# Performance work log

Hardware: AMD Instinct MI355X
Metric: run time of the kernel (lower is better)

Reference implementation:

```python
import jax, jax.numpy as jnp
import numpy as np

B, T, D, H = 64, 128, 256, 256


def setup_inputs() -> dict:
    key = jax.random.key(0)
    k1, k2, k3, k4, k5 = jax.random.split(key, 5)
    inputs = jax.random.normal(k1, (B, T, D), dtype=jnp.float32)
    conditions = jax.random.uniform(k2, (B, T, T), dtype=jnp.float32)
    # Keras GRUCell params (reset_after=True): kernel [D,3H], recurrent_kernel [H,3H], bias [2,3H]
    scale_k = 1.0 / np.sqrt(D)
    scale_r = 1.0 / np.sqrt(H)
    kernel = jax.random.normal(k3, (D, 3 * H), dtype=jnp.float32) * scale_k
    recurrent_kernel = jax.random.normal(k4, (H, 3 * H), dtype=jnp.float32) * scale_r
    bias = jax.random.normal(k5, (2, 3 * H), dtype=jnp.float32) * 0.01
    return {"inputs": inputs, "conditions": conditions, "kernel": kernel,
            "recurrent_kernel": recurrent_kernel, "bias": bias}


def _gru_cell(x, h, kernel, recurrent_kernel, bias):
    # Keras GRUCell, reset_after=True, gate order (z, r, h)
    mx = x @ kernel + bias[0]              # [B, 3H]
    mh = h @ recurrent_kernel + bias[1]    # [B, 3H]
    xz, xr, xh = jnp.split(mx, 3, axis=-1)
    hz, hr, hh = jnp.split(mh, 3, axis=-1)
    z = jax.nn.sigmoid(xz + hz)
    r = jax.nn.sigmoid(xr + hr)
    cand = jnp.tanh(xh + r * hh)
    return z * h + (1.0 - z) * cand


def reference(inputs, conditions, kernel, recurrent_kernel, bias):
    # inputs: [B,T,D]; conditions: [B,T,T]
    x_t = jnp.transpose(inputs, (1, 0, 2))  # [T, B, D]
    units = recurrent_kernel.shape[0]
    b, t = inputs.shape[0], inputs.shape[1]

    def step(outs, i):
        # outs: [T, B, H] outputs so far (zeros for future steps, matching TF TensorArray)
        # next_state[b,:] = sum_j conditions[b,i,j] * outs[j,b,:]
        h_prev = jnp.einsum('bj,jbh->bh', conditions[:, i, :], outs)
        h = _gru_cell(x_t[i], h_prev, kernel, recurrent_kernel, bias)
        outs = outs.at[i].set(h)
        return outs, h

    outs0 = jnp.zeros((t, b, units), dtype=inputs.dtype)
    _, ys = jax.lax.scan(step, outs0, jnp.arange(t))  # ys: [T, B, H]
    return jnp.transpose(ys, (1, 0, 2))  # return_sequences=True -> [B, T, H]
```

## Files before the change

### kernel.cpp

```cpp
#include <hip/hip_runtime.h>
#include <math.h>

#define B 64
#define T 128
#define D 256
#define H 256
#define G3 768

__global__ __launch_bounds__(256) void mx_gemm_kernel(const float* __restrict__ x,
                                                      const float* __restrict__ K,
                                                      const float* __restrict__ bias,
                                                      float* __restrict__ MX) {
    __shared__ float xt[16][D];
    const int r0 = blockIdx.x * 16;
    const int tid = threadIdx.x;

    for (int idx = tid; idx < 16 * D; idx += 256) {
        xt[idx >> 8][idx & 255] = x[(size_t)(r0 + (idx >> 8)) * D + (idx & 255)];
    }
    __syncthreads();

    float acc0[16], acc1[16], acc2[16];
#pragma unroll
    for (int r = 0; r < 16; ++r) { acc0[r] = 0.f; acc1[r] = 0.f; acc2[r] = 0.f; }

    for (int d = 0; d < D; ++d) {
        float k0 = K[(size_t)d * G3 + tid];
        float k1 = K[(size_t)d * G3 + 256 + tid];
        float k2 = K[(size_t)d * G3 + 512 + tid];
#pragma unroll
        for (int r = 0; r < 16; ++r) {
            float xv = xt[r][d];
            acc0[r] += xv * k0;
            acc1[r] += xv * k1;
            acc2[r] += xv * k2;
        }
    }

    float b0 = bias[tid], b1 = bias[256 + tid], b2 = bias[512 + tid];
    for (int r = 0; r < 16; ++r) {
        size_t row = (size_t)(r0 + r) * G3;
        MX[row + tid]       = acc0[r] + b0;
        MX[row + 256 + tid] = acc1[r] + b1;
        MX[row + 512 + tid] = acc2[r] + b2;
    }
}

__global__ __launch_bounds__(1024) void rnn_kernel(const float* __restrict__ cond,
                                                   const float* __restrict__ MX,
                                                   const float* __restrict__ R,
                                                   const float* __restrict__ bias,
                                                   float* __restrict__ out) {
    const int b = blockIdx.x;
    const int tid = threadIdx.x;

    __shared__ float c_row[T];
    __shared__ float hprev[H];
    __shared__ float mh[G3];
    __shared__ float p1[4][H];
    __shared__ float p2[4][G3];
    __shared__ float bias2[G3];

    if (tid < G3) bias2[tid] = bias[G3 + tid];

    const float* condb = cond + (size_t)b * T * T;
    const float* mxb   = MX   + (size_t)b * T * G3;
    float*       outb  = out  + (size_t)b * T * H;
    const float4* R4   = reinterpret_cast<const float4*>(R);

    const int q  = tid >> 8;
    const int h  = tid & 255;
    const int hq = tid / 192;
    const int cg = tid % 192;

    for (int i = 0; i < T; ++i) {
        if (tid < T) c_row[tid] = condb[(size_t)i * T + tid];
        __syncthreads();

        const int len = (i + 3) >> 2;
        const int j0 = q * len;
        const int j1 = min(i, j0 + len);
        float a0 = 0.f, a1 = 0.f, a2 = 0.f, a3 = 0.f;
        int j = j0;
        for (; j + 3 < j1; j += 4) {
            a0 += c_row[j]     * outb[(size_t)(j)     * H + h];
            a1 += c_row[j + 1] * outb[(size_t)(j + 1) * H + h];
            a2 += c_row[j + 2] * outb[(size_t)(j + 2) * H + h];
            a3 += c_row[j + 3] * outb[(size_t)(j + 3) * H + h];
        }
        for (; j < j1; ++j) a0 += c_row[j] * outb[(size_t)j * H + h];
        p1[q][h] = (a0 + a1) + (a2 + a3);
        __syncthreads();

        float hp = 0.f;
        if (tid < H) {
            hp = p1[0][h] + p1[1][h] + p1[2][h] + p1[3][h];
            hprev[h] = hp;
        }
        __syncthreads();

        if (tid < 768) {
            float4 acc = make_float4(0.f, 0.f, 0.f, 0.f);
            const int h0 = hq * 64;
#pragma unroll 4
            for (int hh = h0; hh < h0 + 64; hh += 4) {
                float4 hp4 = *reinterpret_cast<float4*>(&hprev[hh]);
                float4 r0 = R4[(size_t)(hh + 0) * 192 + cg];
                float4 r1 = R4[(size_t)(hh + 1) * 192 + cg];
                float4 r2 = R4[(size_t)(hh + 2) * 192 + cg];
                float4 r3 = R4[(size_t)(hh + 3) * 192 + cg];
                acc.x += hp4.x * r0.x + hp4.y * r1.x + hp4.z * r2.x + hp4.w * r3.x;
                acc.y += hp4.x * r0.y + hp4.y * r1.y + hp4.z * r2.y + hp4.w * r3.y;
                acc.z += hp4.x * r0.z + hp4.y * r1.z + hp4.z * r2.z + hp4.w * r3.z;
                acc.w += hp4.x * r0.w + hp4.y * r1.w + hp4.z * r2.w + hp4.w * r3.w;
            }
            *reinterpret_cast<float4*>(&p2[hq][cg * 4]) = acc;
        }
        __syncthreads();
        if (tid < 768) {
            mh[tid] = p2[0][tid] + p2[1][tid] + p2[2][tid] + p2[3][tid] + bias2[tid];
        }
        __syncthreads();

        if (tid < H) {
            const size_t mrow = (size_t)i * G3;
            const float xz = mxb[mrow + tid];
            const float xr = mxb[mrow + 256 + tid];
            const float xh = mxb[mrow + 512 + tid];
            const float z  = 1.f / (1.f + expf(-(xz + mh[tid])));
            const float r  = 1.f / (1.f + expf(-(xr + mh[256 + tid])));
            const float cand = tanhf(xh + r * mh[512 + tid]);
            outb[(size_t)i * H + tid] = z * hp + (1.f - z) * cand;
        }
    }
}

extern "C" void kernel_launch(void* const* d_in, const int* in_sizes, int n_in,
                              void* d_out, int out_size, void* d_ws, size_t ws_size,
                              hipStream_t stream) {
    const float* inputs     = (const float*)d_in[0];
    const float* conditions = (const float*)d_in[1];
    const float* kern       = (const float*)d_in[2];
    const float* rker       = (const float*)d_in[3];
    const float* bias       = (const float*)d_in[4];
    float* out = (float*)d_out;
    float* MX  = (float*)d_ws;

    mx_gemm_kernel<<<(B * T) / 16, 256, 0, stream>>>(inputs, kern, bias, MX);
    rnn_kernel<<<B, 1024, 0, stream>>>(conditions, MX, rker, bias, out);
}
```

Before: 1.043 ms.

## Keep GRU output history in LDS and prefetch MX before recurrent GEMV

Stores each step's hidden output in a padded, transposed shared-memory history buffer so the condition-weighted sum over past outputs reads LDS instead of global memory. Condition rows are read directly from global instead of being staged, and the MX row loads are hoisted ahead of the recurrent matvec to overlap their latency. The large LDS footprint limits occupancy to one block per CU and must fit the per-CU LDS limit.

```diff
diff --git a/kernel.cpp b/kernel.cpp
--- a/kernel.cpp
+++ b/kernel.cpp
@@ -6,6 +6,7 @@
 #define D 256
 #define H 256
 #define G3 768
+#define HP 130
 
 __global__ __launch_bounds__(256) void mx_gemm_kernel(const float* __restrict__ x,
                                                       const float* __restrict__ K,
@@ -54,14 +55,11 @@
     const int b = blockIdx.x;
     const int tid = threadIdx.x;
 
-    __shared__ float c_row[T];
-    __shared__ float hprev[H];
+    __shared__ float hist[H][HP];
+    __shared__ float p1[4][H];
+    __shared__ __align__(16) float hprev[H];
+    __shared__ float p2[4][G3];
     __shared__ float mh[G3];
-    __shared__ float p1[4][H];
-    __shared__ float p2[4][G3];
-    __shared__ float bias2[G3];
-
-    if (tid < G3) bias2[tid] = bias[G3 + tid];
 
     const float* condb = cond + (size_t)b * T * T;
     const float* mxb   = MX   + (size_t)b * T * G3;
@@ -74,21 +72,21 @@
     const int cg = tid % 192;
 
     for (int i = 0; i < T; ++i) {
-        if (tid < T) c_row[tid] = condb[(size_t)i * T + tid];
         __syncthreads();
 
+        const float* cr = condb + (size_t)i * T;
         const int len = (i + 3) >> 2;
         const int j0 = q * len;
         const int j1 = min(i, j0 + len);
         float a0 = 0.f, a1 = 0.f, a2 = 0.f, a3 = 0.f;
         int j = j0;
         for (; j + 3 < j1; j += 4) {
-            a0 += c_row[j]     * outb[(size_t)(j)     * H + h];
-            a1 += c_row[j + 1] * outb[(size_t)(j + 1) * H + h];
-            a2 += c_row[j + 2] * outb[(size_t)(j + 2) * H + h];
-            a3 += c_row[j + 3] * outb[(size_t)(j + 3) * H + h];
+            a0 += cr[j]     * hist[h][j];
+            a1 += cr[j + 1] * hist[h][j + 1];
+            a2 += cr[j + 2] * hist[h][j + 2];
+            a3 += cr[j + 3] * hist[h][j + 3];
         }
-        for (; j < j1; ++j) a0 += c_row[j] * outb[(size_t)j * H + h];
+        for (; j < j1; ++j) a0 += cr[j] * hist[h][j];
         p1[q][h] = (a0 + a1) + (a2 + a3);
         __syncthreads();
 
@@ -99,38 +97,47 @@
         }
         __syncthreads();
 
+        float xz = 0.f, xr = 0.f, xh = 0.f;
+        if (tid < H) {
+            const float* mrow = mxb + (size_t)i * G3;
+            xz = mrow[tid];
+            xr = mrow[256 + tid];
+            xh = mrow[512 + tid];
+        }
+
         if (tid < 768) {
             float4 acc = make_float4(0.f, 0.f, 0.f, 0.f);
-            const int h0 = hq * 64;
+            const float4* hp4v = reinterpret_cast<const float4*>(&hprev[hq * 64]);
+            const float4* Rrow = R4 + (size_t)(hq * 64) * 192 + cg;
 #pragma unroll 4
-            for (int hh = h0; hh < h0 + 64; hh += 4) {
-                float4 hp4 = *reinterpret_cast<float4*>(&hprev[hh]);
-                float4 r0 = R4[(size_t)(hh + 0) * 192 + cg];
-                float4 r1 = R4[(size_t)(hh + 1) * 192 + cg];
-                float4 r2 = R4[(size_t)(hh + 2) * 192 + cg];
-                float4 r3 = R4[(size_t)(hh + 3) * 192 + cg];
-                acc.x += hp4.x * r0.x + hp4.y * r1.x + hp4.z * r2.x + hp4.w * r3.x;
-                acc.y += hp4.x * r0.y + hp4.y * r1.y + hp4.z * r2.y + hp4.w * r3.y;
-                acc.z += hp4.x * r0.z + hp4.y * r1.z + hp4.z * r2.z + hp4.w * r3.z;
-                acc.w += hp4.x * r0.w + hp4.y * r1.w + hp4.z * r2.w + hp4.w * r3.w;
+            for (int s = 0; s < 16; ++s) {
+                float4 hv = hp4v[s];
+                float4 r0 = Rrow[(size_t)(4 * s + 0) * 192];
+                float4 r1 = Rrow[(size_t)(4 * s + 1) * 192];
+                float4 r2 = Rrow[(size_t)(4 * s + 2) * 192];
+                float4 r3 = Rrow[(size_t)(4 * s + 3) * 192];
+                acc.x += hv.x * r0.x + hv.y * r1.x + hv.z * r2.x + hv.w * r3.x;
+                acc.y += hv.x * r0.y + hv.y * r1.y + hv.z * r2.y + hv.w * r3.y;
+                acc.z += hv.x * r0.z + hv.y * r1.z + hv.z * r2.z + hv.w * r3.z;
+                acc.w += hv.x * r0.w + hv.y * r1.w + hv.z * r2.w + hv.w * r3.w;
             }
             *reinterpret_cast<float4*>(&p2[hq][cg * 4]) = acc;
         }
         __syncthreads();
-        if (tid < 768) {
-            mh[tid] = p2[0][tid] + p2[1][tid] + p2[2][tid] + p2[3][tid] + bias2[tid];
+
+        if (tid < G3) {
+            mh[tid] = p2[0][tid] + p2[1][tid] + p2[2][tid] + p2[3][tid]
+                    + bias[G3 + tid];
         }
         __syncthreads();
 
         if (tid < H) {
-            const size_t mrow = (size_t)i * G3;
-            const float xz = mxb[mrow + tid];
-            const float xr = mxb[mrow + 256 + tid];
-            const float xh = mxb[mrow + 512 + tid];
-            const float z  = 1.f / (1.f + expf(-(xz + mh[tid])));
-            const float r  = 1.f / (1.f + expf(-(xr + mh[256 + tid])));
+            const float z    = 1.f / (1.f + expf(-(xz + mh[tid])));
+            const float r    = 1.f / (1.f + expf(-(xr + mh[256 + tid])));
             const float cand = tanhf(xh + r * mh[512 + tid]);
-            outb[(size_t)i * H + tid] = z * hp + (1.f - z) * cand;
+            const float hnew = z * hp + (1.f - z) * cand;
+            hist[tid][i] = hnew;
+            outb[(size_t)i * H + tid] = hnew;
         }
     }
 }
```

Result: faster. 1.004 ms (-3.8%).
